# Optimization experiments

Hardware: AMD Instinct MI355X
Metric: run time of the kernel (lower is better)

The kernel has to match this reference:

```python
import jax, jax.numpy as jnp
import numpy as np

N = 50000

def gcn_conv(h, W, b, src, dst, n):
    # h: [N, Fin] -> linear transform then normalized scatter-add aggregation
    h = h @ W  # [N, Fout]
    # add self-loops (PyG GCNConv default)
    loop = jnp.arange(n, dtype=src.dtype)
    s = jnp.concatenate([src, loop])
    d = jnp.concatenate([dst, loop])
    # symmetric normalization: deg^{-1/2}[s] * deg^{-1/2}[d], deg over target index
    deg = jax.ops.segment_sum(jnp.ones_like(d, dtype=h.dtype), d, num_segments=n)
    dinv = jnp.where(deg > 0, jax.lax.rsqrt(deg), 0.0)
    norm = dinv[s] * dinv[d]  # [E+N]
    msg = h[s] * norm[:, None]  # gather + scale
    out = jax.ops.segment_sum(msg, d, num_segments=n)  # scatter-add
    return out + b


def setup_inputs() -> dict:
    key = jax.random.key(0)
    k1, k2, k3, k4, k5, k6 = jax.random.split(key, 6)
    Fin, Fh, Fout = 512, 256, 64
    E = 800000
    x = jax.random.normal(k1, (N, Fin), dtype=jnp.float32)
    edge_index = jax.random.randint(k2, (2, E), 0, N, dtype=jnp.int64)
    # Glorot-style init matching nn Parameter scale
    W1 = jax.random.normal(k3, (Fin, Fh), dtype=jnp.float32) * (1.0 / np.sqrt(Fin))
    b1 = jnp.zeros((Fh,), dtype=jnp.float32)
    W2 = jax.random.normal(k4, (Fh, Fout), dtype=jnp.float32) * (1.0 / np.sqrt(Fh))
    b2 = jnp.zeros((Fout,), dtype=jnp.float32)
    return {"x": x, "edge_index": edge_index, "W1": W1, "b1": b1, "W2": W2, "b2": b2}


def reference(x, edge_index, W1, b1, W2, b2):
    src, dst = edge_index[0], edge_index[1]
    h1 = jax.nn.relu(gcn_conv(x, W1, b1, src, dst, N))
    # dropout is identity in eval mode
    h2 = gcn_conv(h1, W2, b2, src, dst, N)
    return jax.nn.log_softmax(h2, axis=1)
```

## Files before the change

kernel.cpp:

```cpp
#include <hip/hip_runtime.h>
#include <hip/hip_bf16.h>

typedef __attribute__((ext_vector_type(8))) short short8;
typedef __attribute__((ext_vector_type(4))) float f32x4;

#define NNODES 50000

__device__ __forceinline__ float b2f(unsigned short s) {
  union { unsigned int u; float f; } c; c.u = ((unsigned int)s) << 16;
  return c.f;
}
__device__ __forceinline__ unsigned short f2b(float f) {
  return __bfloat16_as_ushort(__float2bfloat16(f));
}
__device__ __forceinline__ unsigned int pkcvt(float a, float b) {
  return (unsigned int)f2b(a) | ((unsigned int)f2b(b) << 16);
}

__device__ __forceinline__ void gl_lds16(const void* g, void* l) {
  __builtin_amdgcn_global_load_lds((const __attribute__((address_space(1))) unsigned int*)g,
                                   (__attribute__((address_space(3))) unsigned int*)l, 16, 0, 0);
}

__global__ __launch_bounds__(256) void k_deg(const int* __restrict__ ei, int* __restrict__ deg, int E,
                                             int* __restrict__ rnk,
                                             const float* __restrict__ W1, const float* __restrict__ W2,
                                             unsigned short* __restrict__ w1t, unsigned short* __restrict__ w2t) {
  int idx = blockIdx.x * 256 + threadIdx.x;
  if (idx < E) {
    int r = atomicAdd(&deg[ei[E + idx]], 1);
    rnk[idx] = r;
  }
  if (idx < 256 * 512) { int nn = idx >> 9, kk = idx & 511; w1t[idx] = f2b(W1[kk * 256 + nn]); }
  int i2 = idx - 256 * 512;
  if (i2 >= 0 && i2 < 64 * 256) { int nn = i2 >> 8, kk = i2 & 255; w2t[i2] = f2b(W2[kk * 64 + nn]); }
}

__global__ __launch_bounds__(256) void k_scanA(const int* __restrict__ deg, int* __restrict__ excl,
                                               int* __restrict__ blksum, float* __restrict__ dinv, int n) {
  const int i = blockIdx.x * 256 + threadIdx.x;
  const int lane = threadIdx.x & 63, wid = threadIdx.x >> 6;
  const int v = (i < n) ? deg[i] : 0;
  int x = v;
#pragma unroll
  for (int o = 1; o < 64; o <<= 1) {
    int y = __shfl_up(x, o, 64);
    if (lane >= o) x += y;
  }
  __shared__ int wsum[4];
  if (lane == 63) wsum[wid] = x;
  __syncthreads();
  int woff = 0;
  for (int w = 0; w < wid; ++w) woff += wsum[w];
  const int incl = x + woff;
  if (i < n) {
    excl[i] = incl - v;
    dinv[i] = rsqrtf((float)v + 1.0f);
  }
  if (threadIdx.x == 255) blksum[blockIdx.x] = incl;
}

__global__ __launch_bounds__(256) void k_scanC(const int* __restrict__ excl, const int* __restrict__ blksum,
                                               int* __restrict__ rowptr, int n, int E) {
  const int t = threadIdx.x;
  int partial = 0;
  for (int j = t; j < (int)blockIdx.x; j += 256) partial += blksum[j];
#pragma unroll
  for (int o = 32; o > 0; o >>= 1) partial += __shfl_xor(partial, o, 64);
  __shared__ int ws[4];
  if ((t & 63) == 0) ws[t >> 6] = partial;
  __syncthreads();
  const int off = ws[0] + ws[1] + ws[2] + ws[3];
  const int i = blockIdx.x * 256 + t;
  if (i < n) rowptr[i] = excl[i] + off;
  if (i == 0) rowptr[n] = E;
}

__global__ __launch_bounds__(256) void k_fillx(const int* __restrict__ ei, const int* __restrict__ rowptr,
                                               const int* __restrict__ rnk, int* __restrict__ csr, int E,
                                               const float* __restrict__ x, unsigned short* __restrict__ xb) {
  int idx = blockIdx.x * 256 + threadIdx.x;
  if (idx < E) {
    const int dst = ei[E + idx];
    csr[rowptr[dst] + rnk[idx]] = ei[idx];
  }
  if (idx < (NNODES * 512) / 8) {
    const float4 v0 = *(const float4*)(x + (size_t)idx * 8);
    const float4 v1 = *(const float4*)(x + (size_t)idx * 8 + 4);
    uint4 p;
    p.x = pkcvt(v0.x, v0.y); p.y = pkcvt(v0.z, v0.w);
    p.z = pkcvt(v1.x, v1.y); p.w = pkcvt(v1.z, v1.w);
    *(uint4*)(xb + (size_t)idx * 8) = p;
  }
}

__global__ __launch_bounds__(256) void k_gemm1(const unsigned short* __restrict__ xb,
    const unsigned short* __restrict__ w1t, const float* __restrict__ dinv,
    unsigned short* __restrict__ hs1h) {
  const int M = NNODES, K = 512;
  const int NRB = (NNODES + 127) / 128;
  const int bid = blockIdx.x;
  const int rowblk = (bid >> 5) * 8 + (bid & 7);
  const int colblk = (bid >> 3) & 3;
  if (rowblk >= NRB) return;

  __shared__ unsigned short Ab[2][128][32];
  __shared__ unsigned short Bb[2][64][32];

  const int tid = threadIdx.x;
  const int w = tid >> 6, lane = tid & 63;
  const int sub = lane >> 2;
  const int brow = rowblk * 128, bcol = colblk * 64;
  const int wr = w >> 1, wc = w & 1;
  const int lr = lane & 15, lk = lane >> 4;

  const int swc = ((lane & 3) ^ ((lane >> 3) & 3)) * 8;
  const int rch = (lk ^ ((lr >> 1) & 3)) * 8;

  int gr0 = brow + w * 16 + sub;      if (gr0 >= M) gr0 = M - 1;
  int gr1 = brow + 64 + w * 16 + sub; if (gr1 >= M) gr1 = M - 1;
  const int grB = bcol + w * 16 + sub;

  const unsigned short* a0p = xb + (size_t)gr0 * K + swc;
  const unsigned short* a1p = xb + (size_t)gr1 * K + swc;
  const unsigned short* bp  = w1t + (size_t)grB * K + swc;

  f32x4 acc[4][2] = {};

#define G1_STAGE(BUF, KT) do { \
    gl_lds16(a0p + (KT), &Ab[BUF][w * 16][0]); \
    gl_lds16(a1p + (KT), &Ab[BUF][64 + w * 16][0]); \
    gl_lds16(bp  + (KT), &Bb[BUF][w * 16][0]); \
  } while (0)

  G1_STAGE(0, 0);
  G1_STAGE(1, 32);
  asm volatile("s_waitcnt vmcnt(3)" ::: "memory");
  __builtin_amdgcn_s_barrier();

  for (int s = 0; s < 16; ++s) {
    const int cur = s & 1;
    short8 af[4], bf[2];
#pragma unroll
    for (int m = 0; m < 4; ++m) af[m] = *(const short8*)&Ab[cur][wr * 64 + m * 16 + lr][rch];
#pragma unroll
    for (int n = 0; n < 2; ++n) bf[n] = *(const short8*)&Bb[cur][wc * 32 + n * 16 + lr][rch];
    if (s < 14) {
      asm volatile("s_waitcnt lgkmcnt(0)" ::: "memory");
      __builtin_amdgcn_s_barrier();
      G1_STAGE(cur, (s + 2) * 32);
    }
#pragma unroll
    for (int m = 0; m < 4; ++m)
#pragma unroll
      for (int n = 0; n < 2; ++n)
        acc[m][n] = __builtin_amdgcn_mfma_f32_16x16x32_bf16(af[m], bf[n], acc[m][n], 0, 0, 0);
    if (s < 14)      asm volatile("s_waitcnt vmcnt(3)" ::: "memory");
    else if (s == 14) asm volatile("s_waitcnt vmcnt(0)" ::: "memory");
    if (s < 15) __builtin_amdgcn_s_barrier();
  }
#undef G1_STAGE

#pragma unroll
  for (int m = 0; m < 4; ++m) {
#pragma unroll
    for (int n = 0; n < 2; ++n) {
      const int col = bcol + wc * 32 + n * 16 + lr;
      unsigned short* dsth = hs1h + (size_t)(col >> 7) * ((size_t)NNODES * 128);
      const int cw = col & 127;
#pragma unroll
      for (int j = 0; j < 4; ++j) {
        const int row = brow + wr * 64 + m * 16 + lk * 4 + j;
        if (row < M) dsth[(size_t)row * 128 + cw] = f2b(acc[m][n][j] * dinv[row]);
      }
    }
  }
}

__global__ __launch_bounds__(256) void k_agg1(const int* __restrict__ rowptr,
    const int* __restrict__ csr, const unsigned short* __restrict__ hs1h,
    const float* __restrict__ dinv, const float* __restrict__ b1,
    unsigned short* __restrict__ h1agg) {
  const int half = blockIdx.x & 1;
  const int chunk = blockIdx.x >> 1;
  const int w = threadIdx.x >> 6, lane = threadIdx.x & 63;
  const int d = chunk * 4 + w;
  if (d >= NNODES) return;
  const unsigned short* __restrict__ src = hs1h + (size_t)half * ((size_t)NNODES * 128);
  const int a = rowptr[d], bnd = rowptr[d + 1];

  unsigned int sv = *(const unsigned int*)(src + (size_t)d * 128 + lane * 2);
  float a0 = b2f((unsigned short)(sv & 0xffff));
  float a1 = b2f((unsigned short)(sv >> 16));

  int e = a;
  for (; e + 8 <= bnd; e += 8) {
    int s[8];
#pragma unroll
    for (int j = 0; j < 8; ++j) s[j] = csr[e + j];
    unsigned int v[8];
#pragma unroll
    for (int j = 0; j < 8; ++j) v[j] = *(const unsigned int*)(src + (size_t)s[j] * 128 + lane * 2);
#pragma unroll
    for (int j = 0; j < 8; ++j) {
      a0 += b2f((unsigned short)(v[j] & 0xffff));
      a1 += b2f((unsigned short)(v[j] >> 16));
    }
  }
  for (; e + 2 <= bnd; e += 2) {
    int s0 = csr[e], s1 = csr[e + 1];
    unsigned int v0 = *(const unsigned int*)(src + (size_t)s0 * 128 + lane * 2);
    unsigned int v1 = *(const unsigned int*)(src + (size_t)s1 * 128 + lane * 2);
    a0 += b2f((unsigned short)(v0 & 0xffff)) + b2f((unsigned short)(v1 & 0xffff));
    a1 += b2f((unsigned short)(v0 >> 16)) + b2f((unsigned short)(v1 >> 16));
  }
  for (; e < bnd; ++e) {
    int s0 = csr[e];
    unsigned int v0 = *(const unsigned int*)(src + (size_t)s0 * 128 + lane * 2);
    a0 += b2f((unsigned short)(v0 & 0xffff));
    a1 += b2f((unsigned short)(v0 >> 16));
  }

  const float di = dinv[d];
  const float2 bb = *(const float2*)(b1 + half * 128 + lane * 2);
  a0 = fmaxf(0.f, a0 * di + bb.x);
  a1 = fmaxf(0.f, a1 * di + bb.y);
  *(unsigned int*)(h1agg + (size_t)half * ((size_t)NNODES * 128) + (size_t)d * 128 + lane * 2) =
      pkcvt(a0, a1);
}

__global__ __launch_bounds__(256) void k_gemm2(const unsigned short* __restrict__ h1agg,
    const unsigned short* __restrict__ w2t, const float* __restrict__ dinv,
    unsigned short* __restrict__ hs2b) {
  const int M = NNODES;
  const size_t HL = (size_t)NNODES * 128;
  const int brow = blockIdx.x * 64;

  __shared__ unsigned short As[2][64][32];
  __shared__ unsigned short Bs[2][64][32];

  const int tid = threadIdx.x;
  const int w = tid >> 6, lane = tid & 63;
  const int sub = lane >> 2;
  const int wr = w >> 1, wc = w & 1;
  const int lr = lane & 15, lk = lane >> 4;

  const int swc = ((lane & 3) ^ ((lane >> 3) & 3)) * 8;
  const int rch = (lk ^ ((lr >> 1) & 3)) * 8;

  int gr = brow + w * 16 + sub; if (gr >= M) gr = M - 1;
  const unsigned short* ap = h1agg + (size_t)gr * 128 + swc;
  const unsigned short* bp = w2t + (size_t)(w * 16 + sub) * 256 + swc;

  f32x4 acc[2][2] = {};

#define G2_STAGE(BUF, S) do { \
    gl_lds16(ap + (size_t)((S) >> 2) * HL + ((S) & 3) * 32, &As[BUF][w * 16][0]); \
    gl_lds16(bp + (S) * 32,                                  &Bs[BUF][w * 16][0]); \
  } while (0)

  G2_STAGE(0, 0);
  G2_STAGE(1, 1);
  asm volatile("s_waitcnt vmcnt(2)" ::: "memory");
  __builtin_amdgcn_s_barrier();

  for (int s = 0; s < 8; ++s) {
    const int cur = s & 1;
    short8 af[2], bf[2];
#pragma unroll
    for (int m = 0; m < 2; ++m) af[m] = *(const short8*)&As[cur][wr * 32 + m * 16 + lr][rch];
#pragma unroll
    for (int n = 0; n < 2; ++n) bf[n] = *(const short8*)&Bs[cur][wc * 32 + n * 16 + lr][rch];
    if (s < 6) {
      asm volatile("s_waitcnt lgkmcnt(0)" ::: "memory");
      __builtin_amdgcn_s_barrier();
      G2_STAGE(cur, s + 2);
    }
#pragma unroll
    for (int m = 0; m < 2; ++m)
#pragma unroll
      for (int n = 0; n < 2; ++n)
        acc[m][n] = __builtin_amdgcn_mfma_f32_16x16x32_bf16(af[m], bf[n], acc[m][n], 0, 0, 0);
    if (s < 6)      asm volatile("s_waitcnt vmcnt(2)" ::: "memory");
    else if (s == 6) asm volatile("s_waitcnt vmcnt(0)" ::: "memory");
    if (s < 7) __builtin_amdgcn_s_barrier();
  }
#undef G2_STAGE

#pragma unroll
  for (int m = 0; m < 2; ++m) {
#pragma unroll
    for (int n = 0; n < 2; ++n) {
      const int col = wc * 32 + n * 16 + lr;
#pragma unroll
      for (int j = 0; j < 4; ++j) {
        const int row = brow + wr * 32 + m * 16 + lk * 4 + j;
        if (row < M) hs2b[(size_t)row * 64 + col] = f2b(acc[m][n][j] * dinv[row]);
      }
    }
  }
}

__global__ __launch_bounds__(256) void k_agg2f(const int* __restrict__ rowptr,
    const int* __restrict__ csr, const unsigned short* __restrict__ hs2b,
    const float* __restrict__ dinv, const float* __restrict__ b2,
    float* __restrict__ out) {
  const int d = blockIdx.x * 4 + (threadIdx.x >> 6);
  if (d >= NNODES) return;
  const int lane = threadIdx.x & 63;
  const int a = rowptr[d], bnd = rowptr[d + 1];

  float acc = b2f(hs2b[(size_t)d * 64 + lane]);

  int i = a;
  for (; i + 16 <= bnd; i += 16) {
    int s[16];
#pragma unroll
    for (int j = 0; j < 16; ++j) s[j] = csr[i + j];
    unsigned short v[16];
#pragma unroll
    for (int j = 0; j < 16; ++j) v[j] = hs2b[(size_t)s[j] * 64 + lane];
#pragma unroll
    for (int j = 0; j < 16; ++j) acc += b2f(v[j]);
  }
  for (; i + 4 <= bnd; i += 4) {
    int s[4];
#pragma unroll
    for (int j = 0; j < 4; ++j) s[j] = csr[i + j];
    unsigned short v[4];
#pragma unroll
    for (int j = 0; j < 4; ++j) v[j] = hs2b[(size_t)s[j] * 64 + lane];
#pragma unroll
    for (int j = 0; j < 4; ++j) acc += b2f(v[j]);
  }
  for (; i < bnd; ++i) acc += b2f(hs2b[(size_t)csr[i] * 64 + lane]);

  float v = acc * dinv[d] + b2[lane];
  float m = v;
#pragma unroll
  for (int o = 32; o > 0; o >>= 1) m = fmaxf(m, __shfl_xor(m, o, 64));
  float ex = expf(v - m);
  float s = ex;
#pragma unroll
  for (int o = 32; o > 0; o >>= 1) s += __shfl_xor(s, o, 64);
  out[(size_t)d * 64 + lane] = v - m - logf(s);
}

extern "C" void kernel_launch(void* const* d_in, const int* in_sizes, int n_in,
                              void* d_out, int out_size, void* d_ws, size_t ws_size,
                              hipStream_t stream) {
  const float* x  = (const float*)d_in[0];
  const int*   ei = (const int*)d_in[1];
  const float* W1 = (const float*)d_in[2];
  const float* b1 = (const float*)d_in[3];
  const float* W2 = (const float*)d_in[4];
  const float* b2 = (const float*)d_in[5];
  float* out = (float*)d_out;
  const int E = in_sizes[1] / 2;
  const int n = NNODES;
  const int nblk = (n + 255) / 256;

  char* ws = (char*)d_ws;
  size_t off = 0;
  auto alloc = [&](size_t bytes) { char* p = ws + off; off = (off + bytes + 255) & ~(size_t)255; return p; };
  int*            deg    = (int*)alloc((size_t)n * 4);
  float*          dinv   = (float*)alloc((size_t)n * 4);
  int*            excl   = (int*)alloc((size_t)n * 4);
  int*            blksum = (int*)alloc((size_t)nblk * 4);
  int*            rowptr = (int*)alloc((size_t)(n + 1) * 4);
  int*            rnk    = (int*)alloc((size_t)E * 4);
  int*            csr    = (int*)alloc((size_t)E * 4);
  unsigned short* w1t    = (unsigned short*)alloc(256 * 512 * 2);
  unsigned short* w2t    = (unsigned short*)alloc(64 * 256 * 2);
  unsigned short* hs1h   = (unsigned short*)alloc((size_t)n * 256 * 2);
  unsigned short* h1agg  = (unsigned short*)alloc((size_t)n * 256 * 2);
  unsigned short* hs2b   = (unsigned short*)alloc((size_t)n * 64 * 2);
  unsigned short* xb     = (unsigned short*)alloc((size_t)n * 512 * 2);
  (void)ws_size; (void)n_in; (void)out_size;

  hipMemsetAsync(deg, 0, (size_t)n * 4, stream);
  k_deg<<<(E + 255) / 256, 256, 0, stream>>>(ei, deg, E, rnk, W1, W2, w1t, w2t);
  k_scanA<<<nblk, 256, 0, stream>>>(deg, excl, blksum, dinv, n);
  k_scanC<<<nblk, 256, 0, stream>>>(excl, blksum, rowptr, n, E);
  k_fillx<<<(NNODES * 512 / 8 + 255) / 256, 256, 0, stream>>>(ei, rowptr, rnk, csr, E, x, xb);
  k_gemm1<<<49 * 32, 256, 0, stream>>>(xb, w1t, dinv, hs1h);
  k_agg1<<<12500 * 2, 256, 0, stream>>>(rowptr, csr, hs1h, dinv, b1, h1agg);
  k_gemm2<<<(n + 63) / 64, 256, 0, stream>>>(h1agg, w2t, dinv, hs2b);
  k_agg2f<<<(n + 3) / 4, 256, 0, stream>>>(rowptr, csr, hs2b, dinv, b2, out);
}
```

Baseline: 220.6 us.

## Split hidden features into eight 32-column slabs for cache-friendly aggregation

The first-layer GEMM output and the aggregated hidden features move from two 128-column halves to eight 32-column slabs. Each aggregation pass then gathers rows of only 64 bytes, and its working set of 3.2 MB per slab fits in L2 better. Each wavefront now splits the edges of a node across four 16-lane groups and combines them with shuffles, and gemm2's staging addresses are updated to the new layout. In exchange, each gather is smaller and less efficient, the CSR indices are read eight times instead of twice, and the reduction adds shuffles.

```diff
diff --git a/kernel.cpp b/kernel.cpp
--- a/kernel.cpp
+++ b/kernel.cpp
@@ -96,7 +96,7 @@
 
 __global__ __launch_bounds__(256) void k_gemm1(const unsigned short* __restrict__ xb,
     const unsigned short* __restrict__ w1t, const float* __restrict__ dinv,
-    unsigned short* __restrict__ hs1h) {
+    unsigned short* __restrict__ hs1cb) {
   const int M = NNODES, K = 512;
   const int NRB = (NNODES + 127) / 128;
   const int bid = blockIdx.x;
@@ -166,74 +166,82 @@
 #pragma unroll
     for (int n = 0; n < 2; ++n) {
       const int col = bcol + wc * 32 + n * 16 + lr;
-      unsigned short* dsth = hs1h + (size_t)(col >> 7) * ((size_t)NNODES * 128);
-      const int cw = col & 127;
+      unsigned short* dst = hs1cb + (size_t)(col >> 5) * ((size_t)NNODES * 32);
+      const int cw = col & 31;
 #pragma unroll
       for (int j = 0; j < 4; ++j) {
         const int row = brow + wr * 64 + m * 16 + lk * 4 + j;
-        if (row < M) dsth[(size_t)row * 128 + cw] = f2b(acc[m][n][j] * dinv[row]);
+        if (row < M) dst[(size_t)row * 32 + cw] = f2b(acc[m][n][j] * dinv[row]);
       }
     }
   }
 }
 
 __global__ __launch_bounds__(256) void k_agg1(const int* __restrict__ rowptr,
-    const int* __restrict__ csr, const unsigned short* __restrict__ hs1h,
+    const int* __restrict__ csr, const unsigned short* __restrict__ hs1cb,
     const float* __restrict__ dinv, const float* __restrict__ b1,
     unsigned short* __restrict__ h1agg) {
-  const int half = blockIdx.x & 1;
-  const int chunk = blockIdx.x >> 1;
+  const int pass = blockIdx.x & 7;
+  const int chunk = blockIdx.x >> 3;
   const int w = threadIdx.x >> 6, lane = threadIdx.x & 63;
-  const int d = chunk * 4 + w;
-  if (d >= NNODES) return;
-  const unsigned short* __restrict__ src = hs1h + (size_t)half * ((size_t)NNODES * 128);
-  const int a = rowptr[d], bnd = rowptr[d + 1];
-
-  unsigned int sv = *(const unsigned int*)(src + (size_t)d * 128 + lane * 2);
-  float a0 = b2f((unsigned short)(sv & 0xffff));
-  float a1 = b2f((unsigned short)(sv >> 16));
-
-  int e = a;
-  for (; e + 8 <= bnd; e += 8) {
-    int s[8];
-#pragma unroll
-    for (int j = 0; j < 8; ++j) s[j] = csr[e + j];
-    unsigned int v[8];
-#pragma unroll
-    for (int j = 0; j < 8; ++j) v[j] = *(const unsigned int*)(src + (size_t)s[j] * 128 + lane * 2);
-#pragma unroll
-    for (int j = 0; j < 8; ++j) {
-      a0 += b2f((unsigned short)(v[j] & 0xffff));
-      a1 += b2f((unsigned short)(v[j] >> 16));
-    }
-  }
-  for (; e + 2 <= bnd; e += 2) {
-    int s0 = csr[e], s1 = csr[e + 1];
-    unsigned int v0 = *(const unsigned int*)(src + (size_t)s0 * 128 + lane * 2);
-    unsigned int v1 = *(const unsigned int*)(src + (size_t)s1 * 128 + lane * 2);
-    a0 += b2f((unsigned short)(v0 & 0xffff)) + b2f((unsigned short)(v1 & 0xffff));
-    a1 += b2f((unsigned short)(v0 >> 16)) + b2f((unsigned short)(v1 >> 16));
-  }
-  for (; e < bnd; ++e) {
-    int s0 = csr[e];
-    unsigned int v0 = *(const unsigned int*)(src + (size_t)s0 * 128 + lane * 2);
-    a0 += b2f((unsigned short)(v0 & 0xffff));
-    a1 += b2f((unsigned short)(v0 >> 16));
-  }
-
-  const float di = dinv[d];
-  const float2 bb = *(const float2*)(b1 + half * 128 + lane * 2);
-  a0 = fmaxf(0.f, a0 * di + bb.x);
-  a1 = fmaxf(0.f, a1 * di + bb.y);
-  *(unsigned int*)(h1agg + (size_t)half * ((size_t)NNODES * 128) + (size_t)d * 128 + lane * 2) =
-      pkcvt(a0, a1);
+  const int g = lane >> 4;
+  const int cl = lane & 15;
+  const size_t SL = (size_t)NNODES * 32;
+  const unsigned short* __restrict__ src = hs1cb + (size_t)pass * SL;
+  const float2 bb = *(const float2*)(b1 + pass * 32 + cl * 2);
+
+  for (int i = 0; i < 4; ++i) {
+    const int d = chunk * 16 + w * 4 + i;
+    if (d >= NNODES) return;
+    const int a = rowptr[d], bnd = rowptr[d + 1];
+    float a0 = 0.f, a1 = 0.f;
+    if (g == 0) {
+      unsigned int sv = *(const unsigned int*)(src + (size_t)d * 32 + cl * 2);
+      a0 = b2f((unsigned short)(sv & 0xffff));
+      a1 = b2f((unsigned short)(sv >> 16));
+    }
+    int e = a;
+    for (; e + 16 <= bnd; e += 16) {
+      int s[4];
+#pragma unroll
+      for (int j = 0; j < 4; ++j) s[j] = csr[e + g + 4 * j];
+      unsigned int v[4];
+#pragma unroll
+      for (int j = 0; j < 4; ++j) v[j] = *(const unsigned int*)(src + (size_t)s[j] * 32 + cl * 2);
+#pragma unroll
+      for (int j = 0; j < 4; ++j) {
+        a0 += b2f((unsigned short)(v[j] & 0xffff));
+        a1 += b2f((unsigned short)(v[j] >> 16));
+      }
+    }
+    for (; e + 4 <= bnd; e += 4) {
+      int s0 = csr[e + g];
+      unsigned int v = *(const unsigned int*)(src + (size_t)s0 * 32 + cl * 2);
+      a0 += b2f((unsigned short)(v & 0xffff));
+      a1 += b2f((unsigned short)(v >> 16));
+    }
+    if (e + g < bnd) {
+      int s0 = csr[e + g];
+      unsigned int v = *(const unsigned int*)(src + (size_t)s0 * 32 + cl * 2);
+      a0 += b2f((unsigned short)(v & 0xffff));
+      a1 += b2f((unsigned short)(v >> 16));
+    }
+    a0 += __shfl_xor(a0, 16, 64); a0 += __shfl_xor(a0, 32, 64);
+    a1 += __shfl_xor(a1, 16, 64); a1 += __shfl_xor(a1, 32, 64);
+
+    const float di = dinv[d];
+    const float r0 = fmaxf(0.f, a0 * di + bb.x);
+    const float r1 = fmaxf(0.f, a1 * di + bb.y);
+    if (g == 0)
+      *(unsigned int*)(h1agg + (size_t)pass * SL + (size_t)d * 32 + cl * 2) = pkcvt(r0, r1);
+  }
 }
 
 __global__ __launch_bounds__(256) void k_gemm2(const unsigned short* __restrict__ h1agg,
     const unsigned short* __restrict__ w2t, const float* __restrict__ dinv,
     unsigned short* __restrict__ hs2b) {
   const int M = NNODES;
-  const size_t HL = (size_t)NNODES * 128;
+  const size_t SL = (size_t)NNODES * 32;
   const int brow = blockIdx.x * 64;
 
   __shared__ unsigned short As[2][64][32];
@@ -249,14 +257,14 @@
   const int rch = (lk ^ ((lr >> 1) & 3)) * 8;
 
   int gr = brow + w * 16 + sub; if (gr >= M) gr = M - 1;
-  const unsigned short* ap = h1agg + (size_t)gr * 128 + swc;
+  const unsigned short* ap = h1agg + (size_t)gr * 32 + swc;
   const unsigned short* bp = w2t + (size_t)(w * 16 + sub) * 256 + swc;
 
   f32x4 acc[2][2] = {};
 
 #define G2_STAGE(BUF, S) do { \
-    gl_lds16(ap + (size_t)((S) >> 2) * HL + ((S) & 3) * 32, &As[BUF][w * 16][0]); \
-    gl_lds16(bp + (S) * 32,                                  &Bs[BUF][w * 16][0]); \
+    gl_lds16(ap + (size_t)(S) * SL, &As[BUF][w * 16][0]); \
+    gl_lds16(bp + (S) * 32,         &Bs[BUF][w * 16][0]); \
   } while (0)
 
   G2_STAGE(0, 0);
@@ -372,7 +380,7 @@
   int*            csr    = (int*)alloc((size_t)E * 4);
   unsigned short* w1t    = (unsigned short*)alloc(256 * 512 * 2);
   unsigned short* w2t    = (unsigned short*)alloc(64 * 256 * 2);
-  unsigned short* hs1h   = (unsigned short*)alloc((size_t)n * 256 * 2);
+  unsigned short* hs1cb  = (unsigned short*)alloc((size_t)n * 256 * 2);
   unsigned short* h1agg  = (unsigned short*)alloc((size_t)n * 256 * 2);
   unsigned short* hs2b   = (unsigned short*)alloc((size_t)n * 64 * 2);
   unsigned short* xb     = (unsigned short*)alloc((size_t)n * 512 * 2);
@@ -383,8 +391,8 @@
   k_scanA<<<nblk, 256, 0, stream>>>(deg, excl, blksum, dinv, n);
   k_scanC<<<nblk, 256, 0, stream>>>(excl, blksum, rowptr, n, E);
   k_fillx<<<(NNODES * 512 / 8 + 255) / 256, 256, 0, stream>>>(ei, rowptr, rnk, csr, E, x, xb);
-  k_gemm1<<<49 * 32, 256, 0, stream>>>(xb, w1t, dinv, hs1h);
-  k_agg1<<<12500 * 2, 256, 0, stream>>>(rowptr, csr, hs1h, dinv, b1, h1agg);
+  k_gemm1<<<49 * 32, 256, 0, stream>>>(xb, w1t, dinv, hs1cb);
+  k_agg1<<<3125 * 8, 256, 0, stream>>>(rowptr, csr, hs1cb, dinv, b1, h1agg);
   k_gemm2<<<(n + 63) / 64, 256, 0, stream>>>(h1agg, w2t, dinv, hs2b);
   k_agg2f<<<(n + 3) / 4, 256, 0, stream>>>(rowptr, csr, hs2b, dinv, b2, out);
 }
```

Result: slower. 272.0 us (+23.3%).
